# Optimization experiments

Measured on AMD Instinct MI355X. Metric: run time of the kernel, lower is better.

The kernel has to match this reference:

```python
import jax, jax.numpy as jnp
import numpy as np

NUM_CHANNELS = 256


def setup_inputs() -> dict:
    key = jax.random.key(0)
    k1, k2, k3, k4, k5 = jax.random.split(key, 5)
    shape = (16, NUM_CHANNELS, 128, 128)
    input_gray = jax.random.normal(k1, shape, dtype=jnp.float32)
    input_green = jax.random.normal(k2, shape, dtype=jnp.float32)
    input_rgb = jax.random.normal(k3, shape, dtype=jnp.float32)
    # Conv2d(num_channels, 1, kernel_size=1): weight [1, C, 1, 1] -> flatten to [C], bias [1]
    fan_in = NUM_CHANNELS  # 1x1 kernel
    bound = 1.0 / np.sqrt(fan_in)
    conv_w = jax.random.uniform(k4, (NUM_CHANNELS,), jnp.float32, -bound, bound)
    conv_b = jax.random.uniform(k5, (1,), jnp.float32, -bound, bound)
    return {
        "input_gray": input_gray,
        "input_green": input_green,
        "input_rgb": input_rgb,
        "conv_w": conv_w,
        "conv_b": conv_b,
    }


def _channel_attention(x, conv_w, conv_b):
    # AdaptiveAvgPool2d(1): global mean over H, W -> [B, C]
    pooled = jnp.mean(x, axis=(2, 3))
    # 1x1 conv C -> 1 is a dot over channels: [B]
    logits = jnp.einsum("bc,c->b", pooled, conv_w) + conv_b[0]
    return jax.nn.sigmoid(logits)[:, None, None, None]  # [B,1,1,1]


def reference(input_gray, input_green, input_rgb, conv_w, conv_b):
    fused_gray = input_gray * _channel_attention(input_gray, conv_w, conv_b)
    fused_green = input_green * _channel_attention(input_green, conv_w, conv_b)
    rgb = input_rgb.astype(jnp.float32)
    fused_rgb = rgb * _channel_attention(rgb, conv_w, conv_b)
    # torch.add(a, b, alpha=10) == a + 10*b, applied twice
    return fused_gray + 10.0 * fused_green + 10.0 * fused_rgb
```

## Files before the change

kernel.cpp:

```cpp
#include <hip/hip_runtime.h>
#include <math.h>

#define BATCHES      16
#define CHANNELS     256
#define HW           (128 * 128)
#define PER_BATCH    (CHANNELS * HW)
#define VEC_PER_BATCH (PER_BATCH / 4)
#define BLOCKS_PER_BN 64
#define RTHREADS      256
#define VEC_PER_THREAD (VEC_PER_BATCH / (BLOCKS_PER_BN * RTHREADS))

#define PARTIALS_OFF 0
#define ATT_OFF      (3 * BATCHES * BLOCKS_PER_BN)

__global__ __launch_bounds__(RTHREADS) void fusion_reduce_kernel(
    const float* __restrict__ gray,
    const float* __restrict__ green,
    const float* __restrict__ rgb,
    const float* __restrict__ conv_w,
    float* __restrict__ partials)
{
    int blk   = blockIdx.x;
    int chunk = blk & (BLOCKS_PER_BN - 1);
    int bn    = blk >> 6;
    int batch = bn & (BATCHES - 1);
    int which = bn >> 4;

    const float* x = (which == 0) ? gray : (which == 1) ? green : rgb;
    const float4* xv = reinterpret_cast<const float4*>(x) +
                       (size_t)batch * VEC_PER_BATCH;

    __shared__ float sw[CHANNELS];
    for (int i = threadIdx.x; i < CHANNELS; i += RTHREADS) sw[i] = conv_w[i];
    __syncthreads();

    float sum = 0.0f;
    int base = chunk * (RTHREADS * VEC_PER_THREAD);
    #pragma unroll 4
    for (int i = 0; i < VEC_PER_THREAD; ++i) {
        int v = base + i * RTHREADS + (int)threadIdx.x;
        float4 d = xv[v];
        float wc = sw[v >> 12];
        sum += (d.x + d.y + d.z + d.w) * wc;
    }

    #pragma unroll
    for (int off = 32; off > 0; off >>= 1) sum += __shfl_down(sum, off, 64);

    __shared__ float s4[RTHREADS / 64];
    int wid = threadIdx.x >> 6;
    if ((threadIdx.x & 63) == 0) s4[wid] = sum;
    __syncthreads();
    if (threadIdx.x == 0) {
        float t = s4[0] + s4[1] + s4[2] + s4[3];
        partials[blk] = t;
    }
}

__global__ __launch_bounds__(64) void fusion_att_kernel(
    const float* __restrict__ partials,
    const float* __restrict__ conv_b,
    float* __restrict__ att)
{
    int row = blockIdx.x;
    float v = partials[row * BLOCKS_PER_BN + (int)threadIdx.x];
    #pragma unroll
    for (int off = 32; off > 0; off >>= 1) v += __shfl_down(v, off, 64);
    if (threadIdx.x == 0) {
        float logit = v * (1.0f / (float)HW) + conv_b[0];
        att[row] = 1.0f / (1.0f + expf(-logit));
    }
}

__global__ __launch_bounds__(RTHREADS) void fusion_apply_kernel(
    const float4* __restrict__ gray,
    const float4* __restrict__ green,
    const float4* __restrict__ rgb,
    const float* __restrict__ att,
    float4* __restrict__ out)
{
    size_t i = (size_t)blockIdx.x * RTHREADS + threadIdx.x;
    int b = (int)(i >> 20);
    float ag  = att[b];
    float agr = att[BATCHES + b];
    float ar  = att[2 * BATCHES + b];

    float4 dg = gray[i], dn = green[i], dr = rgb[i];
    float4 o;
    o.x = dg.x * ag + 10.0f * (dn.x * agr + dr.x * ar);
    o.y = dg.y * ag + 10.0f * (dn.y * agr + dr.y * ar);
    o.z = dg.z * ag + 10.0f * (dn.z * agr + dr.z * ar);
    o.w = dg.w * ag + 10.0f * (dn.w * agr + dr.w * ar);
    out[i] = o;
}

extern "C" void kernel_launch(void* const* d_in, const int* in_sizes, int n_in,
                              void* d_out, int out_size, void* d_ws, size_t ws_size,
                              hipStream_t stream) {
    const float* gray   = (const float*)d_in[0];
    const float* green  = (const float*)d_in[1];
    const float* rgb    = (const float*)d_in[2];
    const float* conv_w = (const float*)d_in[3];
    const float* conv_b = (const float*)d_in[4];
    float* out = (float*)d_out;
    float* ws  = (float*)d_ws;

    float* partials = ws + PARTIALS_OFF;
    float* att      = ws + ATT_OFF;

    fusion_reduce_kernel<<<3 * BATCHES * BLOCKS_PER_BN, RTHREADS, 0, stream>>>(
        gray, green, rgb, conv_w, partials);

    fusion_att_kernel<<<3 * BATCHES, 64, 0, stream>>>(partials, conv_b, att);

    int total_vec = BATCHES * VEC_PER_BATCH;
    fusion_apply_kernel<<<total_vec / RTHREADS, RTHREADS, 0, stream>>>(
        (const float4*)gray, (const float4*)green, (const float4*)rgb,
        att, (float4*)out);
}
```

Before: 321.6 us.

## Split reduction into many small one-channel blocks and use nontemporal output stores

```diff
diff --git a/kernel.cpp b/kernel.cpp
--- a/kernel.cpp
+++ b/kernel.cpp
@@ -6,12 +6,16 @@
 #define HW           (128 * 128)
 #define PER_BATCH    (CHANNELS * HW)
 #define VEC_PER_BATCH (PER_BATCH / 4)
-#define BLOCKS_PER_BN 64
 #define RTHREADS      256
-#define VEC_PER_THREAD (VEC_PER_BATCH / (BLOCKS_PER_BN * RTHREADS))
+
+#define K1_BLOCKS     49152
+#define VECS_PER_K1   1024
+#define PARTS_PER_ROW 1024
 
 #define PARTIALS_OFF 0
-#define ATT_OFF      (3 * BATCHES * BLOCKS_PER_BN)
+#define ATT_OFF      K1_BLOCKS
+
+typedef float f32x4 __attribute__((ext_vector_type(4)));
 
 __global__ __launch_bounds__(RTHREADS) void fusion_reduce_kernel(
     const float* __restrict__ gray,
@@ -20,29 +24,24 @@
     const float* __restrict__ conv_w,
     float* __restrict__ partials)
 {
-    int blk   = blockIdx.x;
-    int chunk = blk & (BLOCKS_PER_BN - 1);
-    int bn    = blk >> 6;
-    int batch = bn & (BATCHES - 1);
-    int which = bn >> 4;
+    int g     = blockIdx.x;
+    int which = g >> 14;
+    int inner = g & 16383;
+    size_t base = (size_t)inner * VECS_PER_K1;
 
     const float* x = (which == 0) ? gray : (which == 1) ? green : rgb;
-    const float4* xv = reinterpret_cast<const float4*>(x) +
-                       (size_t)batch * VEC_PER_BATCH;
+    const float4* xv = reinterpret_cast<const float4*>(x) + base;
 
-    __shared__ float sw[CHANNELS];
-    for (int i = threadIdx.x; i < CHANNELS; i += RTHREADS) sw[i] = conv_w[i];
-    __syncthreads();
+    float w = conv_w[(int)((base >> 12) & (CHANNELS - 1))];
 
-    float sum = 0.0f;
-    int base = chunk * (RTHREADS * VEC_PER_THREAD);
-    #pragma unroll 4
-    for (int i = 0; i < VEC_PER_THREAD; ++i) {
-        int v = base + i * RTHREADS + (int)threadIdx.x;
-        float4 d = xv[v];
-        float wc = sw[v >> 12];
-        sum += (d.x + d.y + d.z + d.w) * wc;
-    }
+    float4 d0 = xv[threadIdx.x + 0 * RTHREADS];
+    float4 d1 = xv[threadIdx.x + 1 * RTHREADS];
+    float4 d2 = xv[threadIdx.x + 2 * RTHREADS];
+    float4 d3 = xv[threadIdx.x + 3 * RTHREADS];
+    float sum = ((d0.x + d0.y) + (d0.z + d0.w))
+              + ((d1.x + d1.y) + (d1.z + d1.w))
+              + ((d2.x + d2.y) + (d2.z + d2.w))
+              + ((d3.x + d3.y) + (d3.z + d3.w));
 
     #pragma unroll
     for (int off = 32; off > 0; off >>= 1) sum += __shfl_down(sum, off, 64);
@@ -52,22 +51,30 @@
     if ((threadIdx.x & 63) == 0) s4[wid] = sum;
     __syncthreads();
     if (threadIdx.x == 0) {
-        float t = s4[0] + s4[1] + s4[2] + s4[3];
-        partials[blk] = t;
+        partials[g] = ((s4[0] + s4[1]) + (s4[2] + s4[3])) * w;
     }
 }
 
-__global__ __launch_bounds__(64) void fusion_att_kernel(
+__global__ __launch_bounds__(RTHREADS) void fusion_att_kernel(
     const float* __restrict__ partials,
     const float* __restrict__ conv_b,
     float* __restrict__ att)
 {
     int row = blockIdx.x;
-    float v = partials[row * BLOCKS_PER_BN + (int)threadIdx.x];
+    const float* p = partials + (size_t)row * PARTS_PER_ROW;
+    float v = p[threadIdx.x + 0 * RTHREADS] + p[threadIdx.x + 1 * RTHREADS]
+            + p[threadIdx.x + 2 * RTHREADS] + p[threadIdx.x + 3 * RTHREADS];
+
     #pragma unroll
     for (int off = 32; off > 0; off >>= 1) v += __shfl_down(v, off, 64);
+
+    __shared__ float s4[RTHREADS / 64];
+    int wid = threadIdx.x >> 6;
+    if ((threadIdx.x & 63) == 0) s4[wid] = v;
+    __syncthreads();
     if (threadIdx.x == 0) {
-        float logit = v * (1.0f / (float)HW) + conv_b[0];
+        float total = (s4[0] + s4[1]) + (s4[2] + s4[3]);
+        float logit = total * (1.0f / (float)HW) + conv_b[0];
         att[row] = 1.0f / (1.0f + expf(-logit));
     }
 }
@@ -86,12 +93,12 @@
     float ar  = att[2 * BATCHES + b];
 
     float4 dg = gray[i], dn = green[i], dr = rgb[i];
-    float4 o;
+    f32x4 o;
     o.x = dg.x * ag + 10.0f * (dn.x * agr + dr.x * ar);
     o.y = dg.y * ag + 10.0f * (dn.y * agr + dr.y * ar);
     o.z = dg.z * ag + 10.0f * (dn.z * agr + dr.z * ar);
     o.w = dg.w * ag + 10.0f * (dn.w * agr + dr.w * ar);
-    out[i] = o;
+    __builtin_nontemporal_store(o, reinterpret_cast<f32x4*>(&out[i]));
 }
 
 extern "C" void kernel_launch(void* const* d_in, const int* in_sizes, int n_in,
@@ -108,10 +115,11 @@
     float* partials = ws + PARTIALS_OFF;
     float* att      = ws + ATT_OFF;
 
-    fusion_reduce_kernel<<<3 * BATCHES * BLOCKS_PER_BN, RTHREADS, 0, stream>>>(
+    fusion_reduce_kernel<<<K1_BLOCKS, RTHREADS, 0, stream>>>(
         gray, green, rgb, conv_w, partials);
 
-    fusion_att_kernel<<<3 * BATCHES, 64, 0, stream>>>(partials, conv_b, att);
+    fusion_att_kernel<<<3 * BATCHES, RTHREADS, 0, stream>>>(
+        partials, conv_b, att);
 
     int total_vec = BATCHES * VEC_PER_BATCH;
     fusion_apply_kernel<<<total_vec / RTHREADS, RTHREADS, 0, stream>>>(
```

New measurement: 312.0 us (median of 2 runs). 1.03x faster.
